# Kernel tuning notes

Hardware: AMD Instinct MI355X
Metric: run time of the kernel (lower is better)

The kernel has to match this reference:

```python
import jax, jax.numpy as jnp
import numpy as np

B, T, I, H, O = 64, 512, 256, 1024, 512
STEPS = 100


def _lstm_cell(x, h, c, Wih, Whh, b):
    # torch gate order: i, f, g, o ; Wih:[4H,in], Whh:[4H,H]
    g = x @ Wih.T + h @ Whh.T + b
    i, f, gg, o = jnp.split(g, 4, axis=-1)
    c = jax.nn.sigmoid(f) * c + jax.nn.sigmoid(i) * jnp.tanh(gg)
    h = jax.nn.sigmoid(o) * jnp.tanh(c)
    return h, c


def setup_inputs() -> dict:
    key = jax.random.key(0)
    ks = jax.random.split(key, 11)
    s = 1.0 / np.sqrt(H)  # torch nn.LSTM init scale
    f32 = jnp.float32
    return {
        "inputs": jax.random.normal(ks[0], (B, T, I), f32),
        "enc_Wih": jax.random.normal(ks[1], (4 * H, I), f32) * s,
        "enc_Whh": jax.random.normal(ks[2], (4 * H, H), f32) * s,
        "enc_bih": jax.random.normal(ks[3], (4 * H,), f32) * s,
        "enc_bhh": jax.random.normal(ks[4], (4 * H,), f32) * s,
        "dec_Wih": jax.random.normal(ks[5], (4 * H, O), f32) * s,
        "dec_Whh": jax.random.normal(ks[6], (4 * H, H), f32) * s,
        "dec_bih": jax.random.normal(ks[7], (4 * H,), f32) * s,
        "dec_bhh": jax.random.normal(ks[8], (4 * H,), f32) * s,
        "fc_W": jax.random.normal(ks[9], (O, H), f32) * s,
        "fc_b": jax.random.normal(ks[10], (O,), f32) * s,
    }


def reference(inputs, enc_Wih, enc_Whh, enc_bih, enc_bhh,
              dec_Wih, dec_Whh, dec_bih, dec_bhh, fc_W, fc_b):
    b_enc = enc_bih + enc_bhh
    b_dec = dec_bih + dec_bhh
    Bz = inputs.shape[0]
    h0 = jnp.zeros((Bz, H), inputs.dtype)
    c0 = jnp.zeros((Bz, H), inputs.dtype)

    # ---- encoder LSTM over time (batch_first input -> scan over T) ----
    def enc_step(carry, x_t):
        h, c = carry
        h, c = _lstm_cell(x_t, h, c, enc_Wih, enc_Whh, b_enc)
        return (h, c), None

    (h, c), _ = jax.lax.scan(enc_step, (h0, c0), inputs.transpose(1, 0, 2))

    def dec_step(carry, _):
        inp, h, c = carry
        h, c = _lstm_cell(inp, h, c, dec_Wih, dec_Whh, b_dec)
        logits = h @ fc_W.T + fc_b                 # [B, O]
        tok = jnp.argmax(logits, axis=-1)          # [B]
        # next decoder input: predicted token index broadcast to feature dim
        nxt = jnp.broadcast_to(tok[:, None].astype(inputs.dtype), (Bz, O))
        return (nxt, h, c), tok

    init_inp = jnp.zeros((Bz, O), inputs.dtype)
    _, toks = jax.lax.scan(dec_step, (init_inp, h, c), None, length=STEPS)
    # toks: [STEPS, B] -> [B, STEPS, 1] to match torch cat of (B,1,1) tokens
    return toks.T[:, :, None].astype(jnp.int64)
```

## Files before the change

### kernel.cpp

```cpp
#include <hip/hip_runtime.h>
#include <cstdint>
#include <cmath>

#define BB 64
#define TT 512
#define NI 256
#define HH 1024
#define NO 512
#define NSTEPS 100
#define KT 64
#define NBLK 256
#define NTHR 512
#define NCTR 64
#define WD2 16384

__device__ unsigned g_arr[(NCTR + 1) * 32];
__device__ __align__(16) float g_hA[HH * BB];
__device__ __align__(16) float g_hB[HH * BB];
__device__ __align__(16) float g_cst[HH * BB];
__device__ __align__(16) float g_dsum[4 * HH];
__device__ __align__(16) float g_logits[NO * BB];
__device__ __align__(16) float g_xt[TT * NI * BB];

__device__ __forceinline__ float sigf(float x) { return 1.0f / (1.0f + expf(-x)); }

__device__ __forceinline__ float2 ldh2(const float* p) {
  unsigned long long u = __hip_atomic_load((const unsigned long long*)p,
                                           __ATOMIC_RELAXED, __HIP_MEMORY_SCOPE_AGENT);
  union { unsigned long long u; float2 f; } c; c.u = u; return c.f;
}
__device__ __forceinline__ float ldc1(const float* p) {
  unsigned u = __hip_atomic_load((const unsigned*)p,
                                 __ATOMIC_RELAXED, __HIP_MEMORY_SCOPE_AGENT);
  union { unsigned u; float f; } c; c.u = u; return c.f;
}
__device__ __forceinline__ void stc1(float* p, float v) {
  union { float f; unsigned u; } c; c.f = v;
  __hip_atomic_store((unsigned*)p, c.u, __ATOMIC_RELAXED, __HIP_MEMORY_SCOPE_AGENT);
}

__device__ __forceinline__ void bar_arrive(int blk) {
  __syncthreads();
  if (threadIdx.x == 0) {
    __hip_atomic_fetch_add(&g_arr[(blk & (NCTR - 1)) * 32], 1u,
                           __ATOMIC_RELAXED, __HIP_MEMORY_SCOPE_AGENT);
  }
}

__device__ __forceinline__ void bar_wait(unsigned n, unsigned* bf) {
  const int ln = threadIdx.x & 63;
  if ((threadIdx.x >> 6) == 0) {
    for (;;) {
      unsigned v = __hip_atomic_load(&g_arr[ln * 32],
                                     __ATOMIC_RELAXED, __HIP_MEMORY_SCOPE_AGENT);
      #pragma unroll
      for (int off = 32; off; off >>= 1) v += __shfl_xor(v, off);
      if (v >= n * NBLK) break;
      __builtin_amdgcn_s_sleep(1);
    }
    if (ln == 0)
      __hip_atomic_store(bf, n, __ATOMIC_RELEASE, __HIP_MEMORY_SCOPE_WORKGROUP);
  } else {
    while (__hip_atomic_load(bf, __ATOMIC_ACQUIRE, __HIP_MEMORY_SCOPE_WORKGROUP) < n)
      __builtin_amdgcn_s_sleep(2);
  }
}

__global__ void reset_counter() {
  if (threadIdx.x <= NCTR) g_arr[threadIdx.x * 32] = 0u;
}

struct RSlot { float4 a, b; };

#define LOADC_X(R, src) \
  { const float* p_ = (src) + (size_t)((8 * wv + lrow) * BB) + lc4 * 4; \
    (R).a = *(const float4*)p_; \
    (R).b = *(const float4*)(p_ + 4 * BB); }

#define LOADC_H(R, src) \
  { const float* p_ = (src) + (size_t)((8 * wv + lrow) * BB) + lc4 * 4; \
    float2 u0_ = ldh2(p_),        u1_ = ldh2(p_ + 2); \
    float2 u2_ = ldh2(p_ + 4*BB), u3_ = ldh2(p_ + 4*BB + 2); \
    (R).a = make_float4(u0_.x, u0_.y, u1_.x, u1_.y); \
    (R).b = make_float4(u2_.x, u2_.y, u3_.x, u3_.y); }

#define STOREC(bufi, R) \
  { float* b_ = &Su[AsW + (bufi) * 512]; \
    *(float4*)&b_[st0] = (R).a; \
    *(float4*)&b_[st1] = (R).b; }

#define FMA_CHUNK(bufi, ch) \
  { const float* ab_ = &Su[AsW + (bufi) * 512 + row2 * 64]; \
    const float* wp_ = &Wall[(ch) * 1024 + wb]; \
    _Pragma("unroll") \
    for (int kk2 = 0; kk2 < 2; ++kk2) { \
      float4 a0 = *(const float4*)(ab_ + kk2 * 64 + a0c); \
      float4 a1 = *(const float4*)(ab_ + kk2 * 64 + a1c); \
      float4 w0 = *(const float4*)(wp_ + kk2 * 64); \
      float4 w1 = *(const float4*)(wp_ + kk2 * 64 + 4); \
      float av_[8] = {a0.x, a0.y, a0.z, a0.w, a1.x, a1.y, a1.z, a1.w}; \
      float wv_[8] = {w0.x, w0.y, w0.z, w0.w, w1.x, w1.y, w1.z, w1.w}; \
      _Pragma("unroll") for (int r = 0; r < 8; ++r) \
        _Pragma("unroll") for (int c = 0; c < 8; ++c) \
          acc[r][c] = fmaf(wv_[r], av_[c], acc[r][c]); \
    } }

#define LOADD2(R, src, ch) \
  { const float* p_ = (src) + (size_t)(((ch) * KT + 8 * wv + 2 * lrow) * BB) + lc4 * 4; \
    float2 u0_ = ldh2(p_),      u1_ = ldh2(p_ + 2); \
    float2 u2_ = ldh2(p_ + BB), u3_ = ldh2(p_ + BB + 2); \
    (R).a = make_float4(u0_.x, u0_.y, u1_.x, u1_.y); \
    (R).b = make_float4(u2_.x, u2_.y, u3_.x, u3_.y); }

#define FMA_D2(R, ch) \
  { const float* wp_ = &Wall[WD2 + (ch) * 256 + wv * 32 + lrow * 4]; \
    float4 w0 = *(const float4*)(wp_); \
    float4 w1 = *(const float4*)(wp_ + 16); \
    float a_[4] = {(R).a.x, (R).a.y, (R).a.z, (R).a.w}; \
    float b2_[4] = {(R).b.x, (R).b.y, (R).b.z, (R).b.w}; \
    float w0_[4] = {w0.x, w0.y, w0.z, w0.w}; \
    float w1_[4] = {w1.x, w1.y, w1.z, w1.w}; \
    _Pragma("unroll") for (int r = 0; r < 4; ++r) \
      _Pragma("unroll") for (int c = 0; c < 4; ++c) { \
        facc[r][c] = fmaf(w0_[r], a_[c], facc[r][c]); \
        facc[r][c] = fmaf(w1_[r], b2_[c], facc[r][c]); \
      } }

#define GPX(q, rt, cb2) Su[(q) * 1156 + (rt) * 68 + (cb2)]

__global__ void __launch_bounds__(NTHR, 1)
seq2seq_kernel(const float* __restrict__ xin,
               const float* __restrict__ eWih, const float* __restrict__ eWhh,
               const float* __restrict__ ebih, const float* __restrict__ ebhh,
               const float* __restrict__ dWih, const float* __restrict__ dWhh,
               const float* __restrict__ dbih, const float* __restrict__ dbhh,
               const float* __restrict__ fcW,  const float* __restrict__ fcb,
               int* __restrict__ out)
{
  __shared__ __align__(16) float Su[9248];
  __shared__ __align__(16) float Wall[20480];
  __shared__ float avals[8][BB];
  __shared__ int   aidx[8][BB];
  __shared__ float ptok[BB];
  __shared__ unsigned bflag;

  const int tid = threadIdx.x;
  const int blk = blockIdx.x;
  unsigned sync_no = 0;

  const int wv  = tid >> 6;
  const int ln  = tid & 63;
  const int hi  = ln >> 5;
  const int l5  = ln & 31;
  const int jl  = ((l5 >> 4) << 1) | hi;
  const int rg  = (l5 >> 3) & 1;
  const int cg  = l5 & 7;
  const int lrow = ln >> 4;
  const int lc4  = ln & 15;
  const int jj2 = (tid >> 6) & 3;
  const int cb  = tid & 63;
  const int j2  = blk * 4 + jj2;
  const int ktd = 4 * wv + lrow;
  const int AsW = wv * 1024;
  const int st0 = lrow * 64 + ((lc4 ^ (lrow >> 1)) << 2);
  const int st1 = (lrow + 4) * 64 + ((lc4 ^ ((lrow >> 1) + 2)) << 2);
  const int row2 = 2 * jl;
  const int a0c = (((cg << 1) ^ jl) << 2);
  const int a1c = ((((cg << 1) | 1) ^ jl) << 2);
  const int wb  = wv * 128 + (((jl << 1) | rg) << 3);

  {
    if (tid == 0) bflag = 0u;
    if (tid < 256) {
      int idx = blk * 256 + tid;
      stc1(&g_hA[idx], 0.0f);
      g_cst[idx] = 0.0f;
    }
    int rr = blk * 16 + (tid >> 5);
    int l32 = tid & 31;
    const float* wrp = dWih + (size_t)rr * NO;
    float s = 0.0f;
    for (int k = l32; k < NO; k += 32) s += wrp[k];
    for (int off = 16; off; off >>= 1) s += __shfl_down(s, off, 32);
    if (l32 == 0) stc1(&g_dsum[rr], s);
    for (size_t w = (size_t)blk * NTHR + tid; w < (size_t)TT * NI * BB;
         w += (size_t)NBLK * NTHR) {
      int k = (int)(w & (NI - 1));
      int t = (int)((w >> 8) & (TT - 1));
      int b = (int)(w >> 17);
      stc1(&g_xt[((size_t)t * NI + k) * BB + b], xin[w]);
    }
    for (int c = 0; c < 16; ++c) {
      const int gr = (c >> 2) * HH + blk * 4 + (c & 3);
      const int rgc = c >> 3, rc = c & 7, half = rc >> 2, q = rc & 3;
      for (int k = tid; k < NI + HH; k += NTHR) {
        const float w = (k < NI) ? eWih[(size_t)gr * NI + k]
                                 : eWhh[(size_t)gr * HH + (k - NI)];
        const int ch = k >> 6, kl = k & 63, wt = kl >> 3, lo = kl & 7;
        Wall[ch * 1024 + wt * 128 + (lo & 1) * 64 +
             ((((lo >> 1) << 1) | rgc) << 3) + half * 4 + q] = w;
      }
    }
  }
  const float be0 = ebih[j2]          + ebhh[j2];
  const float be1 = ebih[HH + j2]     + ebhh[HH + j2];
  const float be2 = ebih[2 * HH + j2] + ebhh[2 * HH + j2];
  const float be3 = ebih[3 * HH + j2] + ebhh[3 * HH + j2];
  bar_arrive(blk); ++sync_no; bar_wait(sync_no, &bflag);

  const float* hc = g_hA;
  float* hn = g_hB;

  RSlot Rs[4];
  LOADC_X(Rs[0], g_xt);
  LOADC_X(Rs[1], g_xt + (size_t)KT * BB);
  LOADC_X(Rs[2], g_xt + (size_t)2 * KT * BB);

  for (int t = 0; t < TT; ++t) {
    float acc[8][8];
    #pragma unroll
    for (int r = 0; r < 8; ++r)
      #pragma unroll
      for (int c = 0; c < 8; ++c) acc[r][c] = 0.0f;

    STOREC(0, Rs[0]);
    STOREC(1, Rs[1]);
    LOADC_X(Rs[3], g_xt + ((size_t)t * NI + 3 * KT) * BB);
    FMA_CHUNK(0, 0);
    bar_wait(sync_no, &bflag);
    STOREC(0, Rs[2]);
    LOADC_H(Rs[0], hc);
    LOADC_H(Rs[1], hc + (size_t)KT * BB);
    FMA_CHUNK(1, 1);
    STOREC(1, Rs[3]);
    LOADC_H(Rs[2], hc + (size_t)2 * KT * BB);
    FMA_CHUNK(0, 2);
    STOREC(0, Rs[0]);
    LOADC_H(Rs[3], hc + (size_t)3 * KT * BB);
    FMA_CHUNK(1, 3);
    for (int cb4 = 0; cb4 < 3; ++cb4) {
      const int cc = 4 + cb4 * 4;
      STOREC(1, Rs[1]); LOADC_H(Rs[0], hc + (size_t)(cc    ) * KT * BB); FMA_CHUNK(0, cc);
      STOREC(0, Rs[2]); LOADC_H(Rs[1], hc + (size_t)(cc + 1) * KT * BB); FMA_CHUNK(1, cc + 1);
      STOREC(1, Rs[3]); LOADC_H(Rs[2], hc + (size_t)(cc + 2) * KT * BB); FMA_CHUNK(0, cc + 2);
      STOREC(0, Rs[0]); LOADC_H(Rs[3], hc + (size_t)(cc + 3) * KT * BB); FMA_CHUNK(1, cc + 3);
    }
    {
      const int tn = (t + 1 < TT) ? t + 1 : t;
      STOREC(1, Rs[1]); LOADC_X(Rs[0], g_xt + (size_t)tn * NI * BB);            FMA_CHUNK(0, 16);
      STOREC(0, Rs[2]); LOADC_X(Rs[1], g_xt + ((size_t)tn * NI + KT) * BB);     FMA_CHUNK(1, 17);
      STOREC(1, Rs[3]); LOADC_X(Rs[2], g_xt + ((size_t)tn * NI + 2 * KT) * BB); FMA_CHUNK(0, 18);
      FMA_CHUNK(1, 19);
    }
    #pragma unroll
    for (int r = 0; r < 8; ++r)
      #pragma unroll
      for (int c = 0; c < 8; ++c) {
        acc[r][c] += __shfl_xor(acc[r][c], 32);
        acc[r][c] += __shfl_xor(acc[r][c], 16);
      }
    __syncthreads();
    if (ln < 16) {
      #pragma unroll
      for (int r = 0; r < 8; ++r) {
        float4 v0 = {acc[r][0], acc[r][1], acc[r][2], acc[r][3]};
        float4 v1 = {acc[r][4], acc[r][5], acc[r][6], acc[r][7]};
        *(float4*)&GPX(wv, rg * 8 + r, cg * 8)     = v0;
        *(float4*)&GPX(wv, rg * 8 + r, cg * 8 + 4) = v1;
      }
    }
    __syncthreads();
    if (tid < 256) {
      float gsum[4];
      #pragma unroll
      for (int g = 0; g < 4; ++g) {
        const int rt = g * 4 + jj2;
        float ssum = 0.0f;
        #pragma unroll
        for (int q = 0; q < 8; ++q) ssum += GPX(q, rt, cb);
        gsum[g] = ssum;
      }
      float pi = gsum[0] + be0;
      float pf = gsum[1] + be1;
      float pg = gsum[2] + be2;
      float po = gsum[3] + be3;
      float co = g_cst[(size_t)j2 * BB + cb];
      float cn = sigf(pf) * co + sigf(pi) * tanhf(pg);
      float hv = sigf(po) * tanhf(cn);
      g_cst[(size_t)j2 * BB + cb] = cn;
      stc1(&hn[(size_t)j2 * BB + cb], hv);
    }
    bar_arrive(blk); ++sync_no;
    { float* tmp = (float*)hc; hc = hn; hn = tmp; }
  }
  if (tid < BB) ptok[tid] = 0.0f;
  bar_wait(sync_no, &bflag);

  LOADC_H(Rs[0], hc);
  LOADC_H(Rs[1], hc + (size_t)KT * BB);
  LOADC_H(Rs[2], hc + (size_t)2 * KT * BB);
  LOADC_H(Rs[3], hc + (size_t)3 * KT * BB);
  for (int c = 0; c < 16; ++c) {
    const int gr = (c >> 2) * HH + blk * 4 + (c & 3);
    const int rgc = c >> 3, rc = c & 7, half = rc >> 2, q = rc & 3;
    for (int k = tid; k < HH; k += NTHR) {
      const float w = dWhh[(size_t)gr * HH + k];
      const int ch = k >> 6, kl = k & 63, wt = kl >> 3, lo = kl & 7;
      Wall[ch * 1024 + wt * 128 + (lo & 1) * 64 +
           ((((lo >> 1) << 1) | rgc) << 3) + half * 4 + q] = w;
    }
  }
  if (blk < 128) {
    for (int k = tid; k < HH; k += NTHR) {
      const int ch = k >> 6, kl = k & 63, wt = kl >> 3, lo = kl & 7;
      const int base = WD2 + ch * 256 + wt * 32 + (lo & 1) * 16 + (lo >> 1) * 4;
      #pragma unroll
      for (int oo = 0; oo < 4; ++oo)
        Wall[base + oo] = fcW[(size_t)(blk * 4 + oo) * HH + k];
    }
  }
  __syncthreads();

  const float bd0 = dbih[j2]          + dbhh[j2];
  const float bd1 = dbih[HH + j2]     + dbhh[HH + j2];
  const float bd2 = dbih[2 * HH + j2] + dbhh[2 * HH + j2];
  const float bd3 = dbih[3 * HH + j2] + dbhh[3 * HH + j2];
  const float ds0 = g_dsum[j2];
  const float ds1 = g_dsum[HH + j2];
  const float ds2 = g_dsum[2 * HH + j2];
  const float ds3 = g_dsum[3 * HH + j2];

  for (int s = 0; s < NSTEPS; ++s) {
    float acc[8][8];
    #pragma unroll
    for (int r = 0; r < 8; ++r)
      #pragma unroll
      for (int c = 0; c < 8; ++c) acc[r][c] = 0.0f;

    STOREC(0, Rs[0]);
    STOREC(1, Rs[1]); LOADC_H(Rs[0], hc + (size_t)4 * KT * BB); FMA_CHUNK(0, 0);
    STOREC(0, Rs[2]); LOADC_H(Rs[1], hc + (size_t)5 * KT * BB); FMA_CHUNK(1, 1);
    STOREC(1, Rs[3]); LOADC_H(Rs[2], hc + (size_t)6 * KT * BB); FMA_CHUNK(0, 2);
    STOREC(0, Rs[0]); LOADC_H(Rs[3], hc + (size_t)7 * KT * BB); FMA_CHUNK(1, 3);
    for (int cb4 = 0; cb4 < 2; ++cb4) {
      const int cc = 4 + cb4 * 4;
      STOREC(1, Rs[1]); LOADC_H(Rs[0], hc + (size_t)(cc + 4) * KT * BB); FMA_CHUNK(0, cc);
      STOREC(0, Rs[2]); LOADC_H(Rs[1], hc + (size_t)(cc + 5) * KT * BB); FMA_CHUNK(1, cc + 1);
      STOREC(1, Rs[3]); LOADC_H(Rs[2], hc + (size_t)(cc + 6) * KT * BB); FMA_CHUNK(0, cc + 2);
      STOREC(0, Rs[0]); LOADC_H(Rs[3], hc + (size_t)(cc + 7) * KT * BB); FMA_CHUNK(1, cc + 3);
    }
    STOREC(1, Rs[1]); FMA_CHUNK(0, 12);
    STOREC(0, Rs[2]); FMA_CHUNK(1, 13);
    STOREC(1, Rs[3]); FMA_CHUNK(0, 14);
    FMA_CHUNK(1, 15);

    #pragma unroll
    for (int r = 0; r < 8; ++r)
      #pragma unroll
      for (int c = 0; c < 8; ++c) {
        acc[r][c] += __shfl_xor(acc[r][c], 32);
        acc[r][c] += __shfl_xor(acc[r][c], 16);
      }
    __syncthreads();
    if (ln < 16) {
      #pragma unroll
      for (int r = 0; r < 8; ++r) {
        float4 v0 = {acc[r][0], acc[r][1], acc[r][2], acc[r][3]};
        float4 v1 = {acc[r][4], acc[r][5], acc[r][6], acc[r][7]};
        *(float4*)&GPX(wv, rg * 8 + r, cg * 8)     = v0;
        *(float4*)&GPX(wv, rg * 8 + r, cg * 8 + 4) = v1;
      }
    }
    __syncthreads();
    if (tid < 256) {
      float gsum[4];
      #pragma unroll
      for (int g = 0; g < 4; ++g) {
        const int rt = g * 4 + jj2;
        float ssum = 0.0f;
        #pragma unroll
        for (int q = 0; q < 8; ++q) ssum += GPX(q, rt, cb);
        gsum[g] = ssum;
      }
      float tk = ptok[cb];
      float pi = gsum[0] + bd0 + tk * ds0;
      float pf = gsum[1] + bd1 + tk * ds1;
      float pg = gsum[2] + bd2 + tk * ds2;
      float po = gsum[3] + bd3 + tk * ds3;
      float co = g_cst[(size_t)j2 * BB + cb];
      float cn = sigf(pf) * co + sigf(pi) * tanhf(pg);
      float hv = sigf(po) * tanhf(cn);
      g_cst[(size_t)j2 * BB + cb] = cn;
      stc1(&hn[(size_t)j2 * BB + cb], hv);
    }
    bar_arrive(blk); ++sync_no; bar_wait(sync_no, &bflag);
    { float* tmp = (float*)hc; hc = hn; hn = tmp; }

    if (blk < 128) {
      float facc[4][4];
      #pragma unroll
      for (int r = 0; r < 4; ++r)
        #pragma unroll
        for (int c = 0; c < 4; ++c) facc[r][c] = 0.0f;

      LOADD2(Rs[0], hc, 0); LOADD2(Rs[1], hc, 1);
      LOADD2(Rs[2], hc, 2); LOADD2(Rs[3], hc, 3);
      for (int cb4 = 0; cb4 < 3; ++cb4) {
        const int cc = cb4 * 4;
        FMA_D2(Rs[0], cc);     LOADD2(Rs[0], hc, cc + 4);
        FMA_D2(Rs[1], cc + 1); LOADD2(Rs[1], hc, cc + 5);
        FMA_D2(Rs[2], cc + 2); LOADD2(Rs[2], hc, cc + 6);
        FMA_D2(Rs[3], cc + 3); LOADD2(Rs[3], hc, cc + 7);
      }
      FMA_D2(Rs[0], 12); FMA_D2(Rs[1], 13); FMA_D2(Rs[2], 14); FMA_D2(Rs[3], 15);

      #pragma unroll
      for (int r = 0; r < 4; ++r) {
        float4 v = {facc[r][0], facc[r][1], facc[r][2], facc[r][3]};
        *(float4*)&Su[ktd * 272 + r * 68 + lc4 * 4] = v;
      }
      __syncthreads();
      if (tid < 256) {
        const int oo = tid >> 6, ob = tid & 63;
        float ssum = 0.0f;
        #pragma unroll
        for (int q = 0; q < 32; ++q) ssum += Su[q * 272 + oo * 68 + ob];
        const int o = blk * 4 + oo;
        stc1(&g_logits[(size_t)o * BB + ob], ssum + fcb[o]);
      }
    }
    LOADC_H(Rs[0], hc);
    LOADC_H(Rs[1], hc + (size_t)KT * BB);
    LOADC_H(Rs[2], hc + (size_t)2 * KT * BB);
    LOADC_H(Rs[3], hc + (size_t)3 * KT * BB);
    bar_arrive(blk); ++sync_no; bar_wait(sync_no, &bflag);

    {
      const int q = tid >> 6, b = tid & 63;
      float bv = -3.402823466e38f; int bo = 0;
      #pragma unroll
      for (int g = 0; g < 4; ++g) {
        float lv[16];
        #pragma unroll
        for (int i = 0; i < 16; ++i)
          lv[i] = ldc1(&g_logits[(size_t)(q * 64 + g * 16 + i) * BB + b]);
        #pragma unroll
        for (int i = 0; i < 16; ++i)
          if (lv[i] > bv) { bv = lv[i]; bo = q * 64 + g * 16 + i; }
      }
      avals[q][b] = bv; aidx[q][b] = bo;
    }
    __syncthreads();
    if (tid < BB) {
      float bv = avals[0][tid]; int bo = aidx[0][tid];
      #pragma unroll
      for (int q = 1; q < 8; ++q)
        if (avals[q][tid] > bv) { bv = avals[q][tid]; bo = aidx[q][tid]; }
      ptok[tid] = (float)bo;
      if (blk == 0) out[(size_t)tid * NSTEPS + s] = bo;
    }
    __syncthreads();
  }
}

extern "C" void kernel_launch(void* const* d_in, const int* in_sizes, int n_in,
                              void* d_out, int out_size, void* d_ws, size_t ws_size,
                              hipStream_t stream) {
  (void)in_sizes; (void)n_in; (void)out_size; (void)d_ws; (void)ws_size;
  const float* xin  = (const float*)d_in[0];
  const float* eWih = (const float*)d_in[1];
  const float* eWhh = (const float*)d_in[2];
  const float* ebih = (const float*)d_in[3];
  const float* ebhh = (const float*)d_in[4];
  const float* dWih = (const float*)d_in[5];
  const float* dWhh = (const float*)d_in[6];
  const float* dbih = (const float*)d_in[7];
  const float* dbhh = (const float*)d_in[8];
  const float* fcW  = (const float*)d_in[9];
  const float* fcb  = (const float*)d_in[10];
  int* out = (int*)d_out;

  reset_counter<<<1, 128, 0, stream>>>();
  seq2seq_kernel<<<NBLK, NTHR, 0, stream>>>(
      xin, eWih, eWhh, ebih, ebhh, dWih, dWhh, dbih, dbhh, fcW, fcb, out);
}
```

Measured before the change: 12.95 ms.

## Feed recurrent GEMM directly from registers, dropping LDS staging of activations

The per-step recurrent matmul no longer stages h/x chunks through shared memory. Each lane now loads its own activation float4s straight from global memory with inline-asm sc1 loads and explicit vmcnt waits. Weights are re-laid out in LDS with an XOR swizzle so each thread computes a 16x4 tile instead of 8x8. This removes the LDS store/load round trip and its syncs from the latency-critical step loop. In exchange it issues more global loads, uses a different register footprint, and relies on hand-placed waitcnt ordering for correctness.

Measured after the change: 31.20 ms. 141% more time.

```diff
diff --git a/kernel.cpp b/kernel.cpp
--- a/kernel.cpp
+++ b/kernel.cpp
@@ -48,17 +48,17 @@
 }
 
 __device__ __forceinline__ void bar_wait(unsigned n, unsigned* bf) {
-  const int ln = threadIdx.x & 63;
+  const int lnw = threadIdx.x & 63;
   if ((threadIdx.x >> 6) == 0) {
     for (;;) {
-      unsigned v = __hip_atomic_load(&g_arr[ln * 32],
+      unsigned v = __hip_atomic_load(&g_arr[lnw * 32],
                                      __ATOMIC_RELAXED, __HIP_MEMORY_SCOPE_AGENT);
       #pragma unroll
       for (int off = 32; off; off >>= 1) v += __shfl_xor(v, off);
       if (v >= n * NBLK) break;
       __builtin_amdgcn_s_sleep(1);
     }
-    if (ln == 0)
+    if (lnw == 0)
       __hip_atomic_store(bf, n, __ATOMIC_RELEASE, __HIP_MEMORY_SCOPE_WORKGROUP);
   } else {
     while (__hip_atomic_load(bf, __ATOMIC_ACQUIRE, __HIP_MEMORY_SCOPE_WORKGROUP) < n)
@@ -72,38 +72,37 @@
 
 struct RSlot { float4 a, b; };
 
-#define LOADC_X(R, src) \
-  { const float* p_ = (src) + (size_t)((8 * wv + lrow) * BB) + lc4 * 4; \
-    (R).a = *(const float4*)p_; \
-    (R).b = *(const float4*)(p_ + 4 * BB); }
-
-#define LOADC_H(R, src) \
-  { const float* p_ = (src) + (size_t)((8 * wv + lrow) * BB) + lc4 * 4; \
-    float2 u0_ = ldh2(p_),        u1_ = ldh2(p_ + 2); \
-    float2 u2_ = ldh2(p_ + 4*BB), u3_ = ldh2(p_ + 4*BB + 2); \
-    (R).a = make_float4(u0_.x, u0_.y, u1_.x, u1_.y); \
-    (R).b = make_float4(u2_.x, u2_.y, u3_.x, u3_.y); }
-
-#define STOREC(bufi, R) \
-  { float* b_ = &Su[AsW + (bufi) * 512]; \
-    *(float4*)&b_[st0] = (R).a; \
-    *(float4*)&b_[st1] = (R).b; }
-
-#define FMA_CHUNK(bufi, ch) \
-  { const float* ab_ = &Su[AsW + (bufi) * 512 + row2 * 64]; \
-    const float* wp_ = &Wall[(ch) * 1024 + wb]; \
-    _Pragma("unroll") \
-    for (int kk2 = 0; kk2 < 2; ++kk2) { \
-      float4 a0 = *(const float4*)(ab_ + kk2 * 64 + a0c); \
-      float4 a1 = *(const float4*)(ab_ + kk2 * 64 + a1c); \
-      float4 w0 = *(const float4*)(wp_ + kk2 * 64); \
-      float4 w1 = *(const float4*)(wp_ + kk2 * 64 + 4); \
-      float av_[8] = {a0.x, a0.y, a0.z, a0.w, a1.x, a1.y, a1.z, a1.w}; \
-      float wv_[8] = {w0.x, w0.y, w0.z, w0.w, w1.x, w1.y, w1.z, w1.w}; \
-      _Pragma("unroll") for (int r = 0; r < 8; ++r) \
-        _Pragma("unroll") for (int c = 0; c < 8; ++c) \
-          acc[r][c] = fmaf(wv_[r], av_[c], acc[r][c]); \
-    } }
+#define LDH(A0, A1, src, ch) { \
+  const float* p_ = (src) + (ch) * 4096 + lanebase; \
+  asm volatile("global_load_dwordx4 %0, %2, off sc1\n\t" \
+               "global_load_dwordx4 %1, %3, off sc1" \
+               : "=&v"(A0), "=&v"(A1) \
+               : "v"(p_), "v"(p_ + BB)); }
+
+#define LDX(A0, A1, src, ch) { \
+  const float* p_ = (src) + (ch) * 4096 + lanebase; \
+  (A0) = *(const float4*)p_; (A1) = *(const float4*)(p_ + BB); }
+
+#define VW(n) { asm volatile("s_waitcnt vmcnt(" #n ")" ::: "memory"); \
+                __builtin_amdgcn_sched_barrier(0); }
+
+#define FMA_CH(ch, A0, A1) { \
+  const float* wp_ = &Wall[(ch) * 1024 + (8 * wv + 2 * lrow) * 16]; \
+  _Pragma("unroll") \
+  for (int e_ = 0; e_ < 2; ++e_) { \
+    const float4 aa_ = e_ ? (A1) : (A0); \
+    const float* wq_ = wp_ + e_ * 16; \
+    float4 w0_ = *(const float4*)&wq_[(0 ^ lrow) << 2]; \
+    float4 w1_ = *(const float4*)&wq_[(1 ^ lrow) << 2]; \
+    float4 w2_ = *(const float4*)&wq_[(2 ^ lrow) << 2]; \
+    float4 w3_ = *(const float4*)&wq_[(3 ^ lrow) << 2]; \
+    float wr_[16] = {w0_.x, w0_.y, w0_.z, w0_.w, w1_.x, w1_.y, w1_.z, w1_.w, \
+                     w2_.x, w2_.y, w2_.z, w2_.w, w3_.x, w3_.y, w3_.z, w3_.w}; \
+    float av_[4] = {aa_.x, aa_.y, aa_.z, aa_.w}; \
+    _Pragma("unroll") for (int r_ = 0; r_ < 16; ++r_) \
+      _Pragma("unroll") for (int c_ = 0; c_ < 4; ++c_) \
+        acc[r_][c_] = fmaf(wr_[r_], av_[c_], acc[r_][c_]); \
+  } }
 
 #define LOADD2(R, src, ch) \
   { const float* p_ = (src) + (size_t)(((ch) * KT + 8 * wv + 2 * lrow) * BB) + lc4 * 4; \
@@ -150,24 +149,13 @@
 
   const int wv  = tid >> 6;
   const int ln  = tid & 63;
-  const int hi  = ln >> 5;
-  const int l5  = ln & 31;
-  const int jl  = ((l5 >> 4) << 1) | hi;
-  const int rg  = (l5 >> 3) & 1;
-  const int cg  = l5 & 7;
   const int lrow = ln >> 4;
   const int lc4  = ln & 15;
   const int jj2 = (tid >> 6) & 3;
   const int cb  = tid & 63;
   const int j2  = blk * 4 + jj2;
   const int ktd = 4 * wv + lrow;
-  const int AsW = wv * 1024;
-  const int st0 = lrow * 64 + ((lc4 ^ (lrow >> 1)) << 2);
-  const int st1 = (lrow + 4) * 64 + ((lc4 ^ ((lrow >> 1) + 2)) << 2);
-  const int row2 = 2 * jl;
-  const int a0c = (((cg << 1) ^ jl) << 2);
-  const int a1c = ((((cg << 1) | 1) ^ jl) << 2);
-  const int wb  = wv * 128 + (((jl << 1) | rg) << 3);
+  const int lanebase = (8 * wv + 2 * lrow) * BB + lc4 * 4;
 
   {
     if (tid == 0) bflag = 0u;
@@ -190,15 +178,13 @@
       int b = (int)(w >> 17);
       stc1(&g_xt[((size_t)t * NI + k) * BB + b], xin[w]);
     }
-    for (int c = 0; c < 16; ++c) {
-      const int gr = (c >> 2) * HH + blk * 4 + (c & 3);
-      const int rgc = c >> 3, rc = c & 7, half = rc >> 2, q = rc & 3;
+    for (int r2 = 0; r2 < 16; ++r2) {
+      const int gr = (r2 >> 2) * HH + blk * 4 + (r2 & 3);
       for (int k = tid; k < NI + HH; k += NTHR) {
         const float w = (k < NI) ? eWih[(size_t)gr * NI + k]
                                  : eWhh[(size_t)gr * HH + (k - NI)];
-        const int ch = k >> 6, kl = k & 63, wt = kl >> 3, lo = kl & 7;
-        Wall[ch * 1024 + wt * 128 + (lo & 1) * 64 +
-             ((((lo >> 1) << 1) | rgc) << 3) + half * 4 + q] = w;
+        const int ch = k >> 6, kl = k & 63;
+        Wall[ch * 1024 + kl * 16 + (((r2 >> 2) ^ ((kl >> 1) & 3)) << 2) + (r2 & 3)] = w;
       }
     }
   }
@@ -211,62 +197,59 @@
   const float* hc = g_hA;
   float* hn = g_hB;
 
-  RSlot Rs[4];
-  LOADC_X(Rs[0], g_xt);
-  LOADC_X(Rs[1], g_xt + (size_t)KT * BB);
-  LOADC_X(Rs[2], g_xt + (size_t)2 * KT * BB);
+  float4 h0a, h0b, h1a, h1b, h2a, h2b, h3a, h3b;
+  float4 x0a, x0b, x1a, x1b, x2a, x2b, x3a, x3b;
+
+  LDX(x0a, x0b, g_xt, 0);
+  LDX(x1a, x1b, g_xt, 1);
+  LDX(x2a, x2b, g_xt, 2);
+  LDX(x3a, x3b, g_xt, 3);
 
   for (int t = 0; t < TT; ++t) {
-    float acc[8][8];
+    float acc[16][4];
     #pragma unroll
-    for (int r = 0; r < 8; ++r)
-      #pragma unroll
-      for (int c = 0; c < 8; ++c) acc[r][c] = 0.0f;
-
-    STOREC(0, Rs[0]);
-    STOREC(1, Rs[1]);
-    LOADC_X(Rs[3], g_xt + ((size_t)t * NI + 3 * KT) * BB);
-    FMA_CHUNK(0, 0);
+    for (int r = 0; r < 16; ++r)
+      #pragma unroll
+      for (int c = 0; c < 4; ++c) acc[r][c] = 0.0f;
+
+    FMA_CH(0, x0a, x0b);
     bar_wait(sync_no, &bflag);
-    STOREC(0, Rs[2]);
-    LOADC_H(Rs[0], hc);
-    LOADC_H(Rs[1], hc + (size_t)KT * BB);
-    FMA_CHUNK(1, 1);
-    STOREC(1, Rs[3]);
-    LOADC_H(Rs[2], hc + (size_t)2 * KT * BB);
-    FMA_CHUNK(0, 2);
-    STOREC(0, Rs[0]);
-    LOADC_H(Rs[3], hc + (size_t)3 * KT * BB);
-    FMA_CHUNK(1, 3);
-    for (int cb4 = 0; cb4 < 3; ++cb4) {
-      const int cc = 4 + cb4 * 4;
-      STOREC(1, Rs[1]); LOADC_H(Rs[0], hc + (size_t)(cc    ) * KT * BB); FMA_CHUNK(0, cc);
-      STOREC(0, Rs[2]); LOADC_H(Rs[1], hc + (size_t)(cc + 1) * KT * BB); FMA_CHUNK(1, cc + 1);
-      STOREC(1, Rs[3]); LOADC_H(Rs[2], hc + (size_t)(cc + 2) * KT * BB); FMA_CHUNK(0, cc + 2);
-      STOREC(0, Rs[0]); LOADC_H(Rs[3], hc + (size_t)(cc + 3) * KT * BB); FMA_CHUNK(1, cc + 3);
-    }
-    {
-      const int tn = (t + 1 < TT) ? t + 1 : t;
-      STOREC(1, Rs[1]); LOADC_X(Rs[0], g_xt + (size_t)tn * NI * BB);            FMA_CHUNK(0, 16);
-      STOREC(0, Rs[2]); LOADC_X(Rs[1], g_xt + ((size_t)tn * NI + KT) * BB);     FMA_CHUNK(1, 17);
-      STOREC(1, Rs[3]); LOADC_X(Rs[2], g_xt + ((size_t)tn * NI + 2 * KT) * BB); FMA_CHUNK(0, 18);
-      FMA_CHUNK(1, 19);
-    }
+    LDH(h0a, h0b, hc, 0); LDH(h1a, h1b, hc, 1);
+    FMA_CH(1, x1a, x1b);
+    LDH(h2a, h2b, hc, 2);
+    FMA_CH(2, x2a, x2b);
+    LDH(h3a, h3b, hc, 3);
+    FMA_CH(3, x3a, x3b);
+    VW(6); FMA_CH(4, h0a, h0b);  LDH(h0a, h0b, hc, 4);
+    VW(6); FMA_CH(5, h1a, h1b);  LDH(h1a, h1b, hc, 5);
+    VW(6); FMA_CH(6, h2a, h2b);  LDH(h2a, h2b, hc, 6);
+    VW(6); FMA_CH(7, h3a, h3b);  LDH(h3a, h3b, hc, 7);
+    VW(6); FMA_CH(8, h0a, h0b);  LDH(h0a, h0b, hc, 8);
+    VW(6); FMA_CH(9, h1a, h1b);  LDH(h1a, h1b, hc, 9);
+    VW(6); FMA_CH(10, h2a, h2b); LDH(h2a, h2b, hc, 10);
+    VW(6); FMA_CH(11, h3a, h3b); LDH(h3a, h3b, hc, 11);
+    VW(6); FMA_CH(12, h0a, h0b); LDH(h0a, h0b, hc, 12);
+    VW(6); FMA_CH(13, h1a, h1b); LDH(h1a, h1b, hc, 13);
+    VW(6); FMA_CH(14, h2a, h2b); LDH(h2a, h2b, hc, 14);
+    VW(6); FMA_CH(15, h3a, h3b); LDH(h3a, h3b, hc, 15);
+    VW(6); FMA_CH(16, h0a, h0b);
+    VW(4); FMA_CH(17, h1a, h1b);
+    VW(2); FMA_CH(18, h2a, h2b);
+    VW(0); FMA_CH(19, h3a, h3b);
+
     #pragma unroll
-    for (int r = 0; r < 8; ++r)
-      #pragma unroll
-      for (int c = 0; c < 8; ++c) {
+    for (int r = 0; r < 16; ++r)
+      #pragma unroll
+      for (int c = 0; c < 4; ++c) {
         acc[r][c] += __shfl_xor(acc[r][c], 32);
         acc[r][c] += __shfl_xor(acc[r][c], 16);
       }
     __syncthreads();
-    if (ln < 16) {
-      #pragma unroll
-      for (int r = 0; r < 8; ++r) {
-        float4 v0 = {acc[r][0], acc[r][1], acc[r][2], acc[r][3]};
-        float4 v1 = {acc[r][4], acc[r][5], acc[r][6], acc[r][7]};
-        *(float4*)&GPX(wv, rg * 8 + r, cg * 8)     = v0;
-        *(float4*)&GPX(wv, rg * 8 + r, cg * 8 + 4) = v1;
+    if (lrow == 0) {
+      #pragma unroll
+      for (int r = 0; r < 16; ++r) {
+        float4 v = {acc[r][0], acc[r][1], acc[r][2], acc[r][3]};
+        *(float4*)&GPX(wv, r, lc4 * 4) = v;
       }
     }
     __syncthreads();
@@ -290,24 +273,30 @@
       g_cst[(size_t)j2 * BB + cb] = cn;
       stc1(&hn[(size_t)j2 * BB + cb], hv);
     }
+    {
+      const int tn = (t + 1 < TT) ? t + 1 : t;
+      const float* xb = g_xt + (size_t)tn * NI * BB;
+      LDX(x0a, x0b, xb, 0);
+      LDX(x1a, x1b, xb, 1);
+      LDX(x2a, x2b, xb, 2);
+      LDX(x3a, x3b, xb, 3);
+    }
     bar_arrive(blk); ++sync_no;
     { float* tmp = (float*)hc; hc = hn; hn = tmp; }
   }
   if (tid < BB) ptok[tid] = 0.0f;
   bar_wait(sync_no, &bflag);
 
-  LOADC_H(Rs[0], hc);
-  LOADC_H(Rs[1], hc + (size_t)KT * BB);
-  LOADC_H(Rs[2], hc + (size_t)2 * KT * BB);
-  LOADC_H(Rs[3], hc + (size_t)3 * KT * BB);
-  for (int c = 0; c < 16; ++c) {
-    const int gr = (c >> 2) * HH + blk * 4 + (c & 3);
-    const int rgc = c >> 3, rc = c & 7, half = rc >> 2, q = rc & 3;
+  LDH(h0a, h0b, hc, 0);
+  LDH(h1a, h1b, hc, 1);
+  LDH(h2a, h2b, hc, 2);
+  LDH(h3a, h3b, hc, 3);
+  for (int r2 = 0; r2 < 16; ++r2) {
+    const int gr = (r2 >> 2) * HH + blk * 4 + (r2 & 3);
     for (int k = tid; k < HH; k += NTHR) {
-      const float w = dWhh[(size_t)gr * HH + k];
-      const int ch = k >> 6, kl = k & 63, wt = kl >> 3, lo = kl & 7;
-      Wall[ch * 1024 + wt * 128 + (lo & 1) * 64 +
-           ((((lo >> 1) << 1) | rgc) << 3) + half * 4 + q] = w;
+      const int ch = k >> 6, kl = k & 63;
+      Wall[ch * 1024 + kl * 16 + (((r2 >> 2) ^ ((kl >> 1) & 3)) << 2) + (r2 & 3)] =
+          dWhh[(size_t)gr * HH + k];
     }
   }
   if (blk < 128) {
@@ -329,46 +318,45 @@
   const float ds1 = g_dsum[HH + j2];
   const float ds2 = g_dsum[2 * HH + j2];
   const float ds3 = g_dsum[3 * HH + j2];
+  RSlot Ds[4];
 
   for (int s = 0; s < NSTEPS; ++s) {
-    float acc[8][8];
+    float acc[16][4];
     #pragma unroll
-    for (int r = 0; r < 8; ++r)
-      #pragma unroll
-      for (int c = 0; c < 8; ++c) acc[r][c] = 0.0f;
-
-    STOREC(0, Rs[0]);
-    STOREC(1, Rs[1]); LOADC_H(Rs[0], hc + (size_t)4 * KT * BB); FMA_CHUNK(0, 0);
-    STOREC(0, Rs[2]); LOADC_H(Rs[1], hc + (size_t)5 * KT * BB); FMA_CHUNK(1, 1);
-    STOREC(1, Rs[3]); LOADC_H(Rs[2], hc + (size_t)6 * KT * BB); FMA_CHUNK(0, 2);
-    STOREC(0, Rs[0]); LOADC_H(Rs[3], hc + (size_t)7 * KT * BB); FMA_CHUNK(1, 3);
-    for (int cb4 = 0; cb4 < 2; ++cb4) {
-      const int cc = 4 + cb4 * 4;
-      STOREC(1, Rs[1]); LOADC_H(Rs[0], hc + (size_t)(cc + 4) * KT * BB); FMA_CHUNK(0, cc);
-      STOREC(0, Rs[2]); LOADC_H(Rs[1], hc + (size_t)(cc + 5) * KT * BB); FMA_CHUNK(1, cc + 1);
-      STOREC(1, Rs[3]); LOADC_H(Rs[2], hc + (size_t)(cc + 6) * KT * BB); FMA_CHUNK(0, cc + 2);
-      STOREC(0, Rs[0]); LOADC_H(Rs[3], hc + (size_t)(cc + 7) * KT * BB); FMA_CHUNK(1, cc + 3);
-    }
-    STOREC(1, Rs[1]); FMA_CHUNK(0, 12);
-    STOREC(0, Rs[2]); FMA_CHUNK(1, 13);
-    STOREC(1, Rs[3]); FMA_CHUNK(0, 14);
-    FMA_CHUNK(1, 15);
+    for (int r = 0; r < 16; ++r)
+      #pragma unroll
+      for (int c = 0; c < 4; ++c) acc[r][c] = 0.0f;
+
+    FMA_CH(0, h0a, h0b); LDH(h0a, h0b, hc, 4);
+    FMA_CH(1, h1a, h1b); LDH(h1a, h1b, hc, 5);
+    FMA_CH(2, h2a, h2b); LDH(h2a, h2b, hc, 6);
+    FMA_CH(3, h3a, h3b); LDH(h3a, h3b, hc, 7);
+    VW(6); FMA_CH(4, h0a, h0b);  LDH(h0a, h0b, hc, 8);
+    VW(6); FMA_CH(5, h1a, h1b);  LDH(h1a, h1b, hc, 9);
+    VW(6); FMA_CH(6, h2a, h2b);  LDH(h2a, h2b, hc, 10);
+    VW(6); FMA_CH(7, h3a, h3b);  LDH(h3a, h3b, hc, 11);
+    VW(6); FMA_CH(8, h0a, h0b);  LDH(h0a, h0b, hc, 12);
+    VW(6); FMA_CH(9, h1a, h1b);  LDH(h1a, h1b, hc, 13);
+    VW(6); FMA_CH(10, h2a, h2b); LDH(h2a, h2b, hc, 14);
+    VW(6); FMA_CH(11, h3a, h3b); LDH(h3a, h3b, hc, 15);
+    VW(6); FMA_CH(12, h0a, h0b);
+    VW(4); FMA_CH(13, h1a, h1b);
+    VW(2); FMA_CH(14, h2a, h2b);
+    VW(0); FMA_CH(15, h3a, h3b);
 
     #pragma unroll
-    for (int r = 0; r < 8; ++r)
-      #pragma unroll
-      for (int c = 0; c < 8; ++c) {
+    for (int r = 0; r < 16; ++r)
+      #pragma unroll
+      for (int c = 0; c < 4; ++c) {
         acc[r][c] += __shfl_xor(acc[r][c], 32);
         acc[r][c] += __shfl_xor(acc[r][c], 16);
       }
     __syncthreads();
-    if (ln < 16) {
-      #pragma unroll
-      for (int r = 0; r < 8; ++r) {
-        float4 v0 = {acc[r][0], acc[r][1], acc[r][2], acc[r][3]};
-        float4 v1 = {acc[r][4], acc[r][5], acc[r][6], acc[r][7]};
-        *(float4*)&GPX(wv, rg * 8 + r, cg * 8)     = v0;
-        *(float4*)&GPX(wv, rg * 8 + r, cg * 8 + 4) = v1;
+    if (lrow == 0) {
+      #pragma unroll
+      for (int r = 0; r < 16; ++r) {
+        float4 v = {acc[r][0], acc[r][1], acc[r][2], acc[r][3]};
+        *(float4*)&GPX(wv, r, lc4 * 4) = v;
       }
     }
     __syncthreads();
@@ -403,16 +391,16 @@
         #pragma unroll
         for (int c = 0; c < 4; ++c) facc[r][c] = 0.0f;
 
-      LOADD2(Rs[0], hc, 0); LOADD2(Rs[1], hc, 1);
-      LOADD2(Rs[2], hc, 2); LOADD2(Rs[3], hc, 3);
+      LOADD2(Ds[0], hc, 0); LOADD2(Ds[1], hc, 1);
+      LOADD2(Ds[2], hc, 2); LOADD2(Ds[3], hc, 3);
       for (int cb4 = 0; cb4 < 3; ++cb4) {
         const int cc = cb4 * 4;
-        FMA_D2(Rs[0], cc);     LOADD2(Rs[0], hc, cc + 4);
-        FMA_D2(Rs[1], cc + 1); LOADD2(Rs[1], hc, cc + 5);
-        FMA_D2(Rs[2], cc + 2); LOADD2(Rs[2], hc, cc + 6);
-        FMA_D2(Rs[3], cc + 3); LOADD2(Rs[3], hc, cc + 7);
-      }
-      FMA_D2(Rs[0], 12); FMA_D2(Rs[1], 13); FMA_D2(Rs[2], 14); FMA_D2(Rs[3], 15);
+        FMA_D2(Ds[0], cc);     LOADD2(Ds[0], hc, cc + 4);
+        FMA_D2(Ds[1], cc + 1); LOADD2(Ds[1], hc, cc + 5);
+        FMA_D2(Ds[2], cc + 2); LOADD2(Ds[2], hc, cc + 6);
+        FMA_D2(Ds[3], cc + 3); LOADD2(Ds[3], hc, cc + 7);
+      }
+      FMA_D2(Ds[0], 12); FMA_D2(Ds[1], 13); FMA_D2(Ds[2], 14); FMA_D2(Ds[3], 15);
 
       #pragma unroll
       for (int r = 0; r < 4; ++r) {
@@ -429,10 +417,10 @@
         stc1(&g_logits[(size_t)o * BB + ob], ssum + fcb[o]);
       }
     }
-    LOADC_H(Rs[0], hc);
-    LOADC_H(Rs[1], hc + (size_t)KT * BB);
-    LOADC_H(Rs[2], hc + (size_t)2 * KT * BB);
-    LOADC_H(Rs[3], hc + (size_t)3 * KT * BB);
+    LDH(h0a, h0b, hc, 0);
+    LDH(h1a, h1b, hc, 1);
+    LDH(h2a, h2b, hc, 2);
+    LDH(h3a, h3b, hc, 3);
     bar_arrive(blk); ++sync_no; bar_wait(sync_no, &bflag);
 
     {
```

## Keep cell state in LDS and use plain vector loads after acquire fence

Applied to the files above, without the earlier changes.

Each block owns the same hidden units across all steps, so its cell state now lives in shared memory instead of a global buffer, removing a global read and write per step. Per-element relaxed atomic loads of h and logits are replaced by ordinary float4 loads, and the grid barrier gains an agent-scope acquire fence so those loads see other blocks' writes. The risk is that plain loads could hit stale cache lines if the fence does not invalidate the relevant caches.

Result: slower. 13.56 ms (+4.7%).

```diff
diff --git a/kernel.cpp b/kernel.cpp
--- a/kernel.cpp
+++ b/kernel.cpp
@@ -17,23 +17,12 @@
 __device__ unsigned g_arr[(NCTR + 1) * 32];
 __device__ __align__(16) float g_hA[HH * BB];
 __device__ __align__(16) float g_hB[HH * BB];
-__device__ __align__(16) float g_cst[HH * BB];
 __device__ __align__(16) float g_dsum[4 * HH];
 __device__ __align__(16) float g_logits[NO * BB];
 __device__ __align__(16) float g_xt[TT * NI * BB];
 
 __device__ __forceinline__ float sigf(float x) { return 1.0f / (1.0f + expf(-x)); }
 
-__device__ __forceinline__ float2 ldh2(const float* p) {
-  unsigned long long u = __hip_atomic_load((const unsigned long long*)p,
-                                           __ATOMIC_RELAXED, __HIP_MEMORY_SCOPE_AGENT);
-  union { unsigned long long u; float2 f; } c; c.u = u; return c.f;
-}
-__device__ __forceinline__ float ldc1(const float* p) {
-  unsigned u = __hip_atomic_load((const unsigned*)p,
-                                 __ATOMIC_RELAXED, __HIP_MEMORY_SCOPE_AGENT);
-  union { unsigned u; float f; } c; c.u = u; return c.f;
-}
 __device__ __forceinline__ void stc1(float* p, float v) {
   union { float f; unsigned u; } c; c.f = v;
   __hip_atomic_store((unsigned*)p, c.u, __ATOMIC_RELAXED, __HIP_MEMORY_SCOPE_AGENT);
@@ -58,6 +47,7 @@
       if (v >= n * NBLK) break;
       __builtin_amdgcn_s_sleep(1);
     }
+    __builtin_amdgcn_fence(__ATOMIC_ACQUIRE, "agent");
     if (ln == 0)
       __hip_atomic_store(bf, n, __ATOMIC_RELEASE, __HIP_MEMORY_SCOPE_WORKGROUP);
   } else {
@@ -79,10 +69,8 @@
 
 #define LOADC_H(R, src) \
   { const float* p_ = (src) + (size_t)((8 * wv + lrow) * BB) + lc4 * 4; \
-    float2 u0_ = ldh2(p_),        u1_ = ldh2(p_ + 2); \
-    float2 u2_ = ldh2(p_ + 4*BB), u3_ = ldh2(p_ + 4*BB + 2); \
-    (R).a = make_float4(u0_.x, u0_.y, u1_.x, u1_.y); \
-    (R).b = make_float4(u2_.x, u2_.y, u3_.x, u3_.y); }
+    (R).a = *(const float4*)p_; \
+    (R).b = *(const float4*)(p_ + 4 * BB); }
 
 #define STOREC(bufi, R) \
   { float* b_ = &Su[AsW + (bufi) * 512]; \
@@ -107,10 +95,8 @@
 
 #define LOADD2(R, src, ch) \
   { const float* p_ = (src) + (size_t)(((ch) * KT + 8 * wv + 2 * lrow) * BB) + lc4 * 4; \
-    float2 u0_ = ldh2(p_),      u1_ = ldh2(p_ + 2); \
-    float2 u2_ = ldh2(p_ + BB), u3_ = ldh2(p_ + BB + 2); \
-    (R).a = make_float4(u0_.x, u0_.y, u1_.x, u1_.y); \
-    (R).b = make_float4(u2_.x, u2_.y, u3_.x, u3_.y); }
+    (R).a = *(const float4*)p_; \
+    (R).b = *(const float4*)(p_ + BB); }
 
 #define FMA_D2(R, ch) \
   { const float* wp_ = &Wall[WD2 + (ch) * 256 + wv * 32 + lrow * 4]; \
@@ -142,6 +128,7 @@
   __shared__ float avals[8][BB];
   __shared__ int   aidx[8][BB];
   __shared__ float ptok[BB];
+  __shared__ float cLDS[4][65];
   __shared__ unsigned bflag;
 
   const int tid = threadIdx.x;
@@ -172,9 +159,8 @@
   {
     if (tid == 0) bflag = 0u;
     if (tid < 256) {
-      int idx = blk * 256 + tid;
-      stc1(&g_hA[idx], 0.0f);
-      g_cst[idx] = 0.0f;
+      stc1(&g_hA[blk * 256 + tid], 0.0f);
+      cLDS[tid >> 6][tid & 63] = 0.0f;
     }
     int rr = blk * 16 + (tid >> 5);
     int l32 = tid & 31;
@@ -284,10 +270,10 @@
       float pf = gsum[1] + be1;
       float pg = gsum[2] + be2;
       float po = gsum[3] + be3;
-      float co = g_cst[(size_t)j2 * BB + cb];
+      float co = cLDS[jj2][cb];
       float cn = sigf(pf) * co + sigf(pi) * tanhf(pg);
       float hv = sigf(po) * tanhf(cn);
-      g_cst[(size_t)j2 * BB + cb] = cn;
+      cLDS[jj2][cb] = cn;
       stc1(&hn[(size_t)j2 * BB + cb], hv);
     }
     bar_arrive(blk); ++sync_no;
@@ -387,10 +373,10 @@
       float pf = gsum[1] + bd1 + tk * ds1;
       float pg = gsum[2] + bd2 + tk * ds2;
       float po = gsum[3] + bd3 + tk * ds3;
-      float co = g_cst[(size_t)j2 * BB + cb];
+      float co = cLDS[jj2][cb];
       float cn = sigf(pf) * co + sigf(pi) * tanhf(pg);
       float hv = sigf(po) * tanhf(cn);
-      g_cst[(size_t)j2 * BB + cb] = cn;
+      cLDS[jj2][cb] = cn;
       stc1(&hn[(size_t)j2 * BB + cb], hv);
     }
     bar_arrive(blk); ++sync_no; bar_wait(sync_no, &bflag);
@@ -443,7 +429,7 @@
         float lv[16];
         #pragma unroll
         for (int i = 0; i < 16; ++i)
-          lv[i] = ldc1(&g_logits[(size_t)(q * 64 + g * 16 + i) * BB + b]);
+          lv[i] = g_logits[(size_t)(q * 64 + g * 16 + i) * BB + b];
         #pragma unroll
         for (int i = 0; i < 16; ++i)
           if (lv[i] > bv) { bv = lv[i]; bo = q * 64 + g * 16 + i; }
```
